# Kernel optimization log

Hardware: AMD Instinct MI355X
Metric: run time of the kernel (lower is better)

Reference implementation:

```python
import jax, jax.numpy as jnp
import numpy as np

B = 65536        # batch
L = 1024         # input_size
K = 16           # filter_size
NUM_CLASSES = 4


def setup_inputs() -> dict:
    key = jax.random.key(0)
    k1, k2, k3, k4 = jax.random.split(key, 4)
    x = jax.random.normal(k1, (B, 1, L), dtype=jnp.float32)
    w = jax.random.normal(k2, (1, 1, K), dtype=jnp.float32) * 0.1
    b = jax.random.normal(k3, (1,), dtype=jnp.float32) * 0.1
    # per-class (lo, hi) intervals, lo <= hi, non-negative so sqrt fallback is real
    ranges = jnp.sort(jax.random.uniform(k4, (NUM_CLASSES, 2), dtype=jnp.float32) * 2.0, axis=1)
    return {"x": x, "w": w, "b": b, "ranges": ranges}


def reference(x, w, b, ranges):
    # Conv1d(1->1, K) + bias, ReLU, MaxPool1d over the full valid length -> [B,1,1]
    y = jax.lax.conv_general_dilated(
        x, w, window_strides=(1,), padding='VALID',
        dimension_numbers=('NCH', 'OIH', 'NCH'))
    y = jnp.maximum(y + b[None, :, None], 0.0)
    v = jnp.max(y, axis=-1, keepdims=True)            # [B,1,1]

    # vectorized replacement of Tensor.apply_(from_ranges_to_output)
    lo = ranges[:, 0]                                  # [4]
    hi = ranges[:, 1]                                  # [4]
    vv = v[..., None]                                  # [B,1,1,1]
    matches = (vv >= lo) & (vv <= hi)                  # [B,1,1,4]
    in_any = jnp.any(matches, axis=-1)                 # [B,1,1]
    first_match = jnp.argmax(matches, axis=-1)         # first i with v in [lo_i,hi_i]

    # fallback: distances (v^2 + bound)^0.5 over interleaved [lo0,hi0,lo1,hi1,...]
    flat_bounds = ranges.reshape(-1)                   # [8]
    dists = jnp.sqrt(vv * vv + flat_bounds)            # [B,1,1,8]
    fallback_label = jnp.argmin(dists, axis=-1) // 2   # [B,1,1]

    out = jnp.where(in_any, first_match, fallback_label).astype(jnp.uint8)
    return out
```

## Files before the change

kernel.cpp:

```cpp
#include <hip/hip_runtime.h>
#include <math.h>

#define BROWS 65536
#define LLEN  1024
#define KW    16
#define NPOS  (LLEN - KW + 1)
#define RPB   4

__device__ __forceinline__ int swz(int g) { return g ^ ((g >> 3) & 7); }

__global__ __launch_bounds__(256, 8) void conv_pool_classify(
    const float* __restrict__ x,
    const float* __restrict__ w,
    const float* __restrict__ bias,
    const float* __restrict__ ranges,
    int* __restrict__ out)
{
    __shared__ float4 lds[RPB][LLEN / 4];

    const int lane = threadIdx.x & 63;
    const int wid  = threadIdx.x >> 6;
    const int row  = blockIdx.x * RPB + wid;
    const float* __restrict__ xr = x + (size_t)row * LLEN;

    float wv[KW];
#pragma unroll
    for (int k = 0; k < KW; ++k) wv[k] = w[k];

#pragma unroll
    for (int s = 0; s < 4; ++s) {
        const int g = 64 * s + lane;
        lds[wid][swz(g)] = *(const float4*)(xr + 4 * g);
    }
    __syncthreads();

    float xv[32];
#pragma unroll
    for (int j = 0; j < 8; ++j) {
        int g = 4 * lane + j;
        if (g > 255) g = 255;
        *(float4*)(&xv[4 * j]) = lds[wid][swz(g)];
    }

    const int own = 16 * lane;
    float vmax = -INFINITY;
#pragma unroll
    for (int p = 0; p < KW; ++p) {
        float acc = 0.0f;
#pragma unroll
        for (int k = 0; k < KW; ++k) acc = fmaf(xv[p + k], wv[k], acc);
        const bool valid = (own + p) < NPOS;
        vmax = valid ? fmaxf(vmax, acc) : vmax;
    }

#pragma unroll
    for (int off = 32; off > 0; off >>= 1)
        vmax = fmaxf(vmax, __shfl_xor(vmax, off, 64));

    if (lane == 0) {
        const float v = fmaxf(vmax + bias[0], 0.0f);

        int label = -1;
#pragma unroll
        for (int j = 0; j < 4; ++j) {
            const float lo = ranges[2 * j];
            const float hi = ranges[2 * j + 1];
            if (label < 0 && v >= lo && v <= hi) label = j;
        }
        if (label < 0) {
            float best = INFINITY;
            int bj = 0;
#pragma unroll
            for (int j = 0; j < 8; ++j) {
                const float d = sqrtf(v * v + ranges[j]);
                if (d < best) { best = d; bj = j; }
            }
            label = bj >> 1;
        }
        out[row] = label;
    }
}

extern "C" void kernel_launch(void* const* d_in, const int* in_sizes, int n_in,
                              void* d_out, int out_size, void* d_ws, size_t ws_size,
                              hipStream_t stream) {
    const float* x      = (const float*)d_in[0];
    const float* w      = (const float*)d_in[1];
    const float* bias   = (const float*)d_in[2];
    const float* ranges = (const float*)d_in[3];
    int* out = (int*)d_out;

    dim3 grid(BROWS / RPB);
    dim3 block(256);
    conv_pool_classify<<<grid, block, 0, stream>>>(x, w, bias, ranges, out);
}
```

Measured before the change: 355.7 us.

## Process multiple rows per wave with register prefetch and nontemporal loads

Result: faster. 343.1 us (-3.6%).

```diff
diff --git a/kernel.cpp b/kernel.cpp
--- a/kernel.cpp
+++ b/kernel.cpp
@@ -6,78 +6,97 @@
 #define KW    16
 #define NPOS  (LLEN - KW + 1)
 #define RPB   4
+#define NBLOCKS 2048
+#define ROWS_PER_WAVE (BROWS / (NBLOCKS * RPB))
+
+typedef float nt_float4 __attribute__((ext_vector_type(4)));
 
 __device__ __forceinline__ int swz(int g) { return g ^ ((g >> 3) & 7); }
 
-__global__ __launch_bounds__(256, 8) void conv_pool_classify(
+__global__ __launch_bounds__(256) void conv_pool_classify(
     const float* __restrict__ x,
     const float* __restrict__ w,
     const float* __restrict__ bias,
     const float* __restrict__ ranges,
     int* __restrict__ out)
 {
-    __shared__ float4 lds[RPB][LLEN / 4];
+    __shared__ nt_float4 lds[RPB][LLEN / 4];
 
     const int lane = threadIdx.x & 63;
     const int wid  = threadIdx.x >> 6;
-    const int row  = blockIdx.x * RPB + wid;
-    const float* __restrict__ xr = x + (size_t)row * LLEN;
+    const int wave = blockIdx.x * RPB + wid;
+    const int row0 = wave * ROWS_PER_WAVE;
 
     float wv[KW];
 #pragma unroll
     for (int k = 0; k < KW; ++k) wv[k] = w[k];
 
+    nt_float4 p[4];
+    {
+        const float* __restrict__ xr = x + (size_t)row0 * LLEN;
 #pragma unroll
-    for (int s = 0; s < 4; ++s) {
-        const int g = 64 * s + lane;
-        lds[wid][swz(g)] = *(const float4*)(xr + 4 * g);
-    }
-    __syncthreads();
-
-    float xv[32];
-#pragma unroll
-    for (int j = 0; j < 8; ++j) {
-        int g = 4 * lane + j;
-        if (g > 255) g = 255;
-        *(float4*)(&xv[4 * j]) = lds[wid][swz(g)];
+        for (int s = 0; s < 4; ++s)
+            p[s] = __builtin_nontemporal_load((const nt_float4*)(xr + 256 * s + 4 * lane));
     }
 
-    const int own = 16 * lane;
-    float vmax = -INFINITY;
-#pragma unroll
-    for (int p = 0; p < KW; ++p) {
-        float acc = 0.0f;
-#pragma unroll
-        for (int k = 0; k < KW; ++k) acc = fmaf(xv[p + k], wv[k], acc);
-        const bool valid = (own + p) < NPOS;
-        vmax = valid ? fmaxf(vmax, acc) : vmax;
-    }
+    for (int it = 0; it < ROWS_PER_WAVE; ++it) {
+        const int row = row0 + it;
 
 #pragma unroll
-    for (int off = 32; off > 0; off >>= 1)
-        vmax = fmaxf(vmax, __shfl_xor(vmax, off, 64));
+        for (int s = 0; s < 4; ++s)
+            lds[wid][swz(64 * s + lane)] = p[s];
 
-    if (lane == 0) {
-        const float v = fmaxf(vmax + bias[0], 0.0f);
+        if (it + 1 < ROWS_PER_WAVE) {
+            const float* __restrict__ xr = x + (size_t)(row + 1) * LLEN;
+#pragma unroll
+            for (int s = 0; s < 4; ++s)
+                p[s] = __builtin_nontemporal_load((const nt_float4*)(xr + 256 * s + 4 * lane));
+        }
 
-        int label = -1;
+        float xv[32];
 #pragma unroll
-        for (int j = 0; j < 4; ++j) {
-            const float lo = ranges[2 * j];
-            const float hi = ranges[2 * j + 1];
-            if (label < 0 && v >= lo && v <= hi) label = j;
+        for (int j = 0; j < 8; ++j) {
+            int g = 4 * lane + j;
+            if (g > 255) g = 255;
+            *(nt_float4*)(&xv[4 * j]) = lds[wid][swz(g)];
         }
-        if (label < 0) {
-            float best = INFINITY;
-            int bj = 0;
+
+        const int own = 16 * lane;
+        float vmax = -INFINITY;
 #pragma unroll
-            for (int j = 0; j < 8; ++j) {
-                const float d = sqrtf(v * v + ranges[j]);
-                if (d < best) { best = d; bj = j; }
+        for (int pp = 0; pp < KW; ++pp) {
+            float acc = 0.0f;
+#pragma unroll
+            for (int k = 0; k < KW; ++k) acc = fmaf(xv[pp + k], wv[k], acc);
+            vmax = ((own + pp) < NPOS) ? fmaxf(vmax, acc) : vmax;
+        }
+
+#pragma unroll
+        for (int off = 32; off > 0; off >>= 1)
+            vmax = fmaxf(vmax, __shfl_xor(vmax, off, 64));
+
+        if (lane == 0) {
+            const float v = fmaxf(vmax + bias[0], 0.0f);
+
+            int label = -1;
+#pragma unroll
+            for (int j = 0; j < 4; ++j) {
+                const float lo = ranges[2 * j];
+                const float hi = ranges[2 * j + 1];
+                if (label < 0 && v >= lo && v <= hi) label = j;
             }
-            label = bj >> 1;
+            if (label < 0) {
+                float best = INFINITY;
+                int bj = 0;
+#pragma unroll
+                for (int j = 0; j < 8; ++j) {
+                    const float d = sqrtf(v * v + ranges[j]);
+                    if (d < best) { best = d; bj = j; }
+                }
+                label = bj >> 1;
+            }
+            out[row] = label;
         }
-        out[row] = label;
     }
 }
 
@@ -90,7 +109,7 @@
     const float* ranges = (const float*)d_in[3];
     int* out = (int*)d_out;
 
-    dim3 grid(BROWS / RPB);
+    dim3 grid(NBLOCKS);
     dim3 block(256);
     conv_pool_classify<<<grid, block, 0, stream>>>(x, w, bias, ranges, out);
 }
```
